# Performance work log

Measured on AMD Instinct MI355X. Metric: run time of the kernel, lower is better.

## Reference

```python
import jax, jax.numpy as jnp
import numpy as np

TOKEN = 40      # half window -> token_len D = 81
STRIDE = 4
NHEAD = 9
EPS = 1e-5
NEG = -1e30


def _tokenize(x):
    # x: [B, L] -> [B, S, D] centered sliding windows, zero padded
    B, L = x.shape
    D = 2 * TOKEN + 1
    S = -(-L // STRIDE)
    xp = jnp.pad(x, ((0, 0), (TOKEN, TOKEN)))
    idx = jnp.arange(S)[:, None] * STRIDE + jnp.arange(D)[None, :]
    return xp[:, idx]


def _pe(S, D):
    pos = jnp.arange(S, dtype=jnp.float32)[:, None]
    div = jnp.exp(-jnp.log(jnp.float32(10000.0)) * jnp.arange(0, D, 2, dtype=jnp.float32) / D)
    ang = pos * div  # [S, ceil(D/2)]
    pe = jnp.zeros((S, D), dtype=jnp.float32)
    pe = pe.at[:, 0::2].set(jnp.sin(ang))
    pe = pe.at[:, 1::2].set(jnp.cos(ang[:, : D // 2]))
    return pe


def _bn(x, g, b, axes):
    # training-mode batch norm over `axes`, channels last
    m = x.mean(axes, keepdims=True)
    v = x.var(axes, keepdims=True)
    return (x - m) / jnp.sqrt(v + EPS) * g + b


def _forward(x, basel, cali_spec, Wq, Wk, Wq2, Wk2, Wv2, Cv, Wo1, Wo2,
             corr_weight, h_weight, corr_map, g1, b1, ff1_w, ff1_b, g2, b2,
             ff2_w, ff2_b, g3, b3, token_v_w, token_v_b, beta1, alpha1, alpha2,
             fc1_w, fc1_b, bnf1_g, bnf1_b, fc2_w, fc2_b, bnf2_g, bnf2_b, fc3_w, fc3_b):
    D = 2 * TOKEN + 1
    dk = D // NHEAD
    # data normalization (load_data_scale semantics)
    xm = jnp.min(x[:, 20:-20])
    xs = jnp.abs(jnp.max(x[:, 20:-20] - xm))
    xn = (x - xm) / xs
    bs = basel[:, ::STRIDE]                      # [B, S]
    tx = _tokenize(xn)                           # [B, S, D]
    B, S, _ = tx.shape
    pe = _pe(S, D)
    tx = tx + pe
    cn = (cali_spec - xm) / xs
    tc = _tokenize(cn) + pe                      # [Bc, S, D]
    Bc = tc.shape[0]

    # ---- branch 2: calibration-spectrum attention over the batch dim ----
    Q2 = jnp.einsum('bse,hed->shbd', tx, Wq2)    # [S,H,B,dk]
    K2 = jnp.einsum('bse,hed->shbd', tx, Wk2)
    V2 = jnp.einsum('bse,hed->shbd', tx, Wv2)
    cK = jnp.einsum('cse,hed->shcd', tc, Wk2)    # [S,H,Bc,dk]
    cV = jnp.einsum('cse,hed->shcd', tc, Wv2)
    Kc = jnp.concatenate([K2, cK], axis=2)       # [S,H,B+Bc,dk]
    Vc = jnp.concatenate([V2, cV], axis=2)
    sc = jnp.einsum('shbd,shkd->shbk', Q2, Kc) / jnp.sqrt(jnp.float32(dk))
    cols = jnp.arange(B + Bc)
    # banded mask: each sample sees only itself among batch columns, all cali columns
    mask = (cols[None, :] >= B) | (cols[None, :] == jnp.arange(B)[:, None])  # [B, B+Bc]
    sc = jnp.where(mask[None, None], sc, NEG)
    A2 = jax.nn.softmax(sc, axis=-1)
    h2 = jnp.einsum('shbk,shkd->bshd', A2, Vc).reshape(B, S, D) @ Wo2  # [B,S,D]

    # ---- branch 1: correlation-map-biased attention over spectral positions ----
    xh = tx + h2
    Qs = jnp.einsum('bse,hed->bhsd', xh, Wq)
    Ks = jnp.einsum('bse,hed->bhsd', xh, Wk)
    Vs = jnp.einsum('bse,hed->bhsd', xh, Wq)     # original uses Wq for V (bug preserved)
    cw = corr_weight[0]
    bias = (corr_map @ Cv) / jnp.sqrt(jnp.float32(S))  # band_num == S
    As = (1.0 - cw) * jnp.einsum('bhsd,bhtd->bhst', Qs, Ks) / jnp.sqrt(jnp.float32(dk)) + cw * bias
    As = jax.nn.softmax(As, axis=-1)
    h1 = jnp.einsum('bhst,bhtd->bshd', As, Vs).reshape(B, S, D) @ Wo1
    hw = h_weight[0]
    att = (1.0 - hw) * h1 + hw * h2

    # ---- SpectrA residual + FF (BatchNorm over channels) ----
    ma = _bn(att + tx, g1, b1, (0, 1))
    f = jax.nn.relu(ma @ ff1_w + ff1_b)
    f = _bn(f, g2, b2, (0, 1))
    f = jax.nn.relu(f @ ff2_w + ff2_b)
    res = _bn(ma + f, g3, b3, (0, 1))

    # ---- ACiNet head ----
    a = (res @ token_v_w + token_v_b) * jax.nn.softmax(res @ beta1, axis=-1)
    a = a.sum(-1)                                # [B, S]
    fea = alpha1[0] * a + alpha2[0] * bs
    h = jax.nn.relu(fea @ fc1_w + fc1_b)
    h = _bn(h, bnf1_g, bnf1_b, (0,))
    h = jax.nn.relu(h @ fc2_w + fc2_b)
    h = _bn(h, bnf2_g, bnf2_b, (0,))
    return jnp.tanh(h @ fc3_w + fc3_b)


def setup_inputs() -> dict:
    key = jax.random.key(0)
    ks = iter(jax.random.split(key, 64))
    def rn(shape, s=0.05):
        return jax.random.normal(next(ks), shape, dtype=jnp.float32) * s
    B, Bc, L = 32, 16, 2048
    D, H, dk, S, FF, FC1, FC2, Y = 81, 9, 9, 512, 256, 512, 256, 4
    f32 = jnp.float32
    return {
        'x': rn((B, L), 1.0), 'basel': rn((B, L), 1.0), 'cali_spec': rn((Bc, L), 1.0),
        'Wq': rn((H, D, dk)), 'Wk': rn((H, D, dk)), 'Wq2': rn((H, D, dk)),
        'Wk2': rn((H, D, dk)), 'Wv2': rn((H, D, dk)),
        'Cv': rn((S, S)), 'Wo1': rn((D, D)), 'Wo2': rn((D, D)),
        'corr_weight': jnp.array([0.2], dtype=f32), 'h_weight': jnp.array([0.8], dtype=f32),
        'corr_map': rn((S, S), 1.0),
        'g1': jnp.ones(D, f32), 'b1': jnp.zeros(D, f32),
        'ff1_w': rn((D, FF)), 'ff1_b': jnp.zeros(FF, f32),
        'g2': jnp.ones(FF, f32), 'b2': jnp.zeros(FF, f32),
        'ff2_w': rn((FF, D)), 'ff2_b': jnp.zeros(D, f32),
        'g3': jnp.ones(D, f32), 'b3': jnp.zeros(D, f32),
        'token_v_w': rn((D, D)), 'token_v_b': jnp.zeros(D, f32),
        'beta1': jnp.ones((D, D), f32),
        'alpha1': jnp.array([0.8], dtype=f32), 'alpha2': jnp.array([0.2], dtype=f32),
        'fc1_w': rn((S, FC1)), 'fc1_b': jnp.zeros(FC1, f32),
        'bnf1_g': jnp.ones(FC1, f32), 'bnf1_b': jnp.zeros(FC1, f32),
        'fc2_w': rn((FC1, FC2)), 'fc2_b': jnp.zeros(FC2, f32),
        'bnf2_g': jnp.ones(FC2, f32), 'bnf2_b': jnp.zeros(FC2, f32),
        'fc3_w': rn((FC2, Y)), 'fc3_b': jnp.zeros(Y, f32),
    }


def reference(x, basel, cali_spec, Wq, Wk, Wq2, Wk2, Wv2, Cv, Wo1, Wo2,
              corr_weight, h_weight, corr_map, g1, b1, ff1_w, ff1_b, g2, b2,
              ff2_w, ff2_b, g3, b3, token_v_w, token_v_b, beta1, alpha1, alpha2,
              fc1_w, fc1_b, bnf1_g, bnf1_b, fc2_w, fc2_b, bnf2_g, bnf2_b, fc3_w, fc3_b):
    return _forward(x, basel, cali_spec, Wq, Wk, Wq2, Wk2, Wv2, Cv, Wo1, Wo2,
                    corr_weight, h_weight, corr_map, g1, b1, ff1_w, ff1_b, g2, b2,
                    ff2_w, ff2_b, g3, b3, token_v_w, token_v_b, beta1, alpha1, alpha2,
                    fc1_w, fc1_b, bnf1_g, bnf1_b, fc2_w, fc2_b, bnf2_g, bnf2_b, fc3_w, fc3_b)
```

## Files before the change

kernel.cpp:

```cpp
#include <hip/hip_runtime.h>
#include <hip/hip_bf16.h>
#include <math.h>

#define EPSV 1e-5f

typedef float vf2 __attribute__((ext_vector_type(2)));
typedef float vf4 __attribute__((ext_vector_type(4)));


__global__ void minmax_part(const float* __restrict__ x, float* __restrict__ part) {
    __shared__ float smin[256], smax[256];
    int tid = threadIdx.x;
    float mn = 1e30f, mx = -1e30f;
    for (int i = blockIdx.x * 256 + tid; i < 32 * 2008; i += 64 * 256) {
        int b = i / 2008, c = i % 2008 + 20;
        float v = x[b * 2048 + c];
        mn = fminf(mn, v); mx = fmaxf(mx, v);
    }
    smin[tid] = mn; smax[tid] = mx; __syncthreads();
    for (int off = 128; off > 0; off >>= 1) {
        if (tid < off) { smin[tid] = fminf(smin[tid], smin[tid + off]); smax[tid] = fmaxf(smax[tid], smax[tid + off]); }
        __syncthreads();
    }
    if (tid == 0) { part[blockIdx.x] = smin[0]; part[64 + blockIdx.x] = smax[0]; }
}

__global__ void minmax_fin(const float* __restrict__ part, float* __restrict__ scal) {
    __shared__ float smn[64], smx[64];
    int tid = threadIdx.x;
    smn[tid] = part[tid]; smx[tid] = part[64 + tid]; __syncthreads();
    for (int off = 32; off > 0; off >>= 1) {
        if (tid < off) { smn[tid] = fminf(smn[tid], smn[tid + off]); smx[tid] = fmaxf(smx[tid], smx[tid + off]); }
        __syncthreads();
    }
    if (tid == 0) { scal[0] = smn[0]; scal[1] = smx[0] - smn[0]; }
}

__global__ void pe_kernel(float* __restrict__ pe) {
    int idx = blockIdx.x * blockDim.x + threadIdx.x;
    if (idx >= 512 * 81) return;
    int d = idx % 81, s = idx / 81;
    int j = d >> 1;
    float dv = __expf(-9.210340371976184f * (2.0f * (float)j) / 81.0f);
    float ang = (float)s * dv;
    pe[idx] = (d & 1) ? cosf(ang) : sinf(ang);
}

__global__ void tokenize_kernel(const float* __restrict__ x, const float* __restrict__ cali,
                                const float* __restrict__ scal, const float* __restrict__ pe,
                                float* __restrict__ txall) {
    int idx = blockIdx.x * blockDim.x + threadIdx.x;
    if (idx >= 48 * 512 * 81) return;
    int d = idx % 81;
    int s = (idx / 81) % 512;
    int r = idx / (81 * 512);
    float xm = scal[0], inv_xs = 1.0f / scal[1];
    int oc = s * 4 + d - 40;
    float val = 0.0f;
    if (oc >= 0 && oc < 2048) {
        float sv = (r < 32) ? x[r * 2048 + oc] : cali[(r - 32) * 2048 + oc];
        val = (sv - xm) * inv_xs;
    }
    txall[idx] = val + pe[s * 81 + d];
}


__global__ __launch_bounds__(512) void qkv2_kernel(const float* __restrict__ txall,
                            const float* __restrict__ Wq2, const float* __restrict__ Wk2,
                            const float* __restrict__ Wv2,
                            float* __restrict__ Q2, float* __restrict__ Kc, float* __restrict__ Vc) {
    __shared__ float rows_[64 * 84];
    __shared__ float Wl[84 * 84];
    int blk = blockIdx.x;
    int t, rb;
    if (blk < 256)      { t = 0; rb = blk; }
    else if (blk < 640) { t = 1; rb = blk - 256; }
    else                { t = 2; rb = blk - 640; }
    int row0 = rb * 64;
    int k = row0 >> 9;
    int s0 = row0 & 511;
    const float* W = (t == 0) ? Wq2 : (t == 1) ? Wk2 : Wv2;
    int tid = threadIdx.x;
    for (int i = tid; i < 64 * 84; i += 512) {
        int c = i % 84;
        rows_[i] = (c < 81) ? txall[(row0 + i / 84) * 81 + c] : 0.0f;
    }
    for (int i = tid; i < 84 * 84; i += 512) {
        int e = i / 84, hd = i % 84;
        Wl[i] = (e < 81 && hd < 81) ? W[(hd / 9) * 729 + e * 9 + (hd % 9)] : 0.0f;
    }
    __syncthreads();
    for (int o = tid; o < 336; o += 512) {
        int r4 = o / 21, cg = o % 21;
        int c0 = cg * 4;
        const float* rp = rows_ + r4 * 4 * 84;
        vf4 acc0 = 0.0f, acc1 = 0.0f, acc2 = 0.0f, acc3 = 0.0f;
        #pragma unroll 7
        for (int e = 0; e < 84; e += 4) {
            vf4 w0 = *(const vf4*)(Wl + (e + 0) * 84 + c0);
            vf4 w1 = *(const vf4*)(Wl + (e + 1) * 84 + c0);
            vf4 w2 = *(const vf4*)(Wl + (e + 2) * 84 + c0);
            vf4 w3 = *(const vf4*)(Wl + (e + 3) * 84 + c0);
            vf4 r0 = *(const vf4*)(rp + e);
            vf4 r1 = *(const vf4*)(rp + 84 + e);
            vf4 r2 = *(const vf4*)(rp + 168 + e);
            vf4 r3 = *(const vf4*)(rp + 252 + e);
            acc0 += r0[0] * w0 + r0[1] * w1 + r0[2] * w2 + r0[3] * w3;
            acc1 += r1[0] * w0 + r1[1] * w1 + r1[2] * w2 + r1[3] * w3;
            acc2 += r2[0] * w0 + r2[1] * w1 + r2[2] * w2 + r2[3] * w3;
            acc3 += r3[0] * w0 + r3[1] * w1 + r3[2] * w2 + r3[3] * w3;
        }
        vf4 av[4] = {acc0, acc1, acc2, acc3};
        #pragma unroll
        for (int cc = 0; cc < 4; cc++) {
            int col = c0 + cc;
            if (col < 81) {
                int h = col / 9, d = col % 9;
                #pragma unroll
                for (int rr = 0; rr < 4; rr++) {
                    int s = s0 + r4 * 4 + rr;
                    if (t == 0)      Q2[((s * 9 + h) * 32 + k) * 9 + d] = av[rr][cc];
                    else if (t == 1) Kc[((s * 9 + h) * 48 + k) * 9 + d] = av[rr][cc];
                    else             Vc[((s * 9 + h) * 48 + k) * 9 + d] = av[rr][cc];
                }
            }
        }
    }
}

__global__ void attn2_kernel(const float* __restrict__ Q2, const float* __restrict__ Kc,
                             const float* __restrict__ Vc, float* __restrict__ tmp2) {
    int tid = blockIdx.x * blockDim.x + threadIdx.x;
    if (tid >= 512 * 9 * 32) return;
    int b = tid & 31;
    int h = (tid >> 5) % 9;
    int s = tid / 288;
    const float* q = Q2 + ((s * 9 + h) * 32 + b) * 9;
    float qr[9];
    const float c2 = 1.4426950408889634f / 3.0f;
    #pragma unroll
    for (int d = 0; d < 9; d++) qr[d] = q[d] * c2;
    const float* Kb = Kc + (s * 9 + h) * 48 * 9;
    const float* Vb = Vc + (s * 9 + h) * 48 * 9;
    float l = 0.0f, outv[9];
    #pragma unroll
    for (int d = 0; d < 9; d++) outv[d] = 0.0f;
    #pragma unroll
    for (int j = 0; j < 17; j++) {
        int k = (j == 0) ? b : 31 + j;
        const float* kp = Kb + k * 9;
        float acc = 0.0f;
        #pragma unroll
        for (int d = 0; d < 9; d++) acc += qr[d] * kp[d];
        float p = exp2f(acc);
        l += p;
        const float* vp = Vb + k * 9;
        #pragma unroll
        for (int d = 0; d < 9; d++) outv[d] += p * vp[d];
    }
    float invl = 1.0f / l;
    float* op = tmp2 + (b * 512 + s) * 81 + h * 9;
    #pragma unroll
    for (int d = 0; d < 9; d++) op[d] = outv[d] * invl;
}

__global__ __launch_bounds__(512) void h2xh_kernel(const float* __restrict__ tmp2,
                            const float* __restrict__ Wo2, const float* __restrict__ txall,
                            float* __restrict__ h2, float* __restrict__ xh) {
    __shared__ float rows_[64 * 84];
    __shared__ float Wl[84 * 84];
    int row0 = blockIdx.x * 64;
    int tid = threadIdx.x;
    for (int i = tid; i < 64 * 84; i += 512) {
        int c = i % 84;
        rows_[i] = (c < 81) ? tmp2[(row0 + i / 84) * 81 + c] : 0.0f;
    }
    for (int i = tid; i < 84 * 84; i += 512) {
        int e = i / 84, c = i % 84;
        Wl[i] = (e < 81 && c < 81) ? Wo2[e * 81 + c] : 0.0f;
    }
    __syncthreads();
    for (int o = tid; o < 336; o += 512) {
        int r4 = o / 21, cg = o % 21;
        int c0 = cg * 4;
        const float* rp = rows_ + r4 * 4 * 84;
        vf4 acc0 = 0.0f, acc1 = 0.0f, acc2 = 0.0f, acc3 = 0.0f;
        #pragma unroll 7
        for (int e = 0; e < 84; e += 4) {
            vf4 w0 = *(const vf4*)(Wl + (e + 0) * 84 + c0);
            vf4 w1 = *(const vf4*)(Wl + (e + 1) * 84 + c0);
            vf4 w2 = *(const vf4*)(Wl + (e + 2) * 84 + c0);
            vf4 w3 = *(const vf4*)(Wl + (e + 3) * 84 + c0);
            vf4 r0 = *(const vf4*)(rp + e);
            vf4 r1 = *(const vf4*)(rp + 84 + e);
            vf4 r2 = *(const vf4*)(rp + 168 + e);
            vf4 r3 = *(const vf4*)(rp + 252 + e);
            acc0 += r0[0] * w0 + r0[1] * w1 + r0[2] * w2 + r0[3] * w3;
            acc1 += r1[0] * w0 + r1[1] * w1 + r1[2] * w2 + r1[3] * w3;
            acc2 += r2[0] * w0 + r2[1] * w1 + r2[2] * w2 + r2[3] * w3;
            acc3 += r3[0] * w0 + r3[1] * w1 + r3[2] * w2 + r3[3] * w3;
        }
        vf4 av[4] = {acc0, acc1, acc2, acc3};
        #pragma unroll
        for (int cc = 0; cc < 4; cc++) {
            int col = c0 + cc;
            if (col < 81) {
                #pragma unroll
                for (int rr = 0; rr < 4; rr++) {
                    int idx = (row0 + r4 * 4 + rr) * 81 + col;
                    float v = av[rr][cc];
                    h2[idx] = v;
                    xh[idx] = txall[idx] + v;
                }
            }
        }
    }
}

__global__ __launch_bounds__(512) void qks_kernel(const float* __restrict__ xh,
                           const float* __restrict__ Wq, const float* __restrict__ Wk,
                           float* __restrict__ Qs, float* __restrict__ Ks) {
    __shared__ float rows_[64 * 84];
    __shared__ float Wl[84 * 84];
    int blk = blockIdx.x;
    int t = blk >> 8;
    int rb = blk & 255;
    int row0 = rb * 64;
    int b = row0 >> 9;
    int s0 = row0 & 511;
    const float* W = (t == 0) ? Wq : Wk;
    int tid = threadIdx.x;
    for (int i = tid; i < 64 * 84; i += 512) {
        int c = i % 84;
        rows_[i] = (c < 81) ? xh[(row0 + i / 84) * 81 + c] : 0.0f;
    }
    for (int i = tid; i < 84 * 84; i += 512) {
        int e = i / 84, hd = i % 84;
        Wl[i] = (e < 81 && hd < 81) ? W[(hd / 9) * 729 + e * 9 + (hd % 9)] : 0.0f;
    }
    __syncthreads();
    float* dst = (t == 0) ? Qs : Ks;
    for (int o = tid; o < 336; o += 512) {
        int r4 = o / 21, cg = o % 21;
        int c0 = cg * 4;
        const float* rp = rows_ + r4 * 4 * 84;
        vf4 acc0 = 0.0f, acc1 = 0.0f, acc2 = 0.0f, acc3 = 0.0f;
        #pragma unroll 7
        for (int e = 0; e < 84; e += 4) {
            vf4 w0 = *(const vf4*)(Wl + (e + 0) * 84 + c0);
            vf4 w1 = *(const vf4*)(Wl + (e + 1) * 84 + c0);
            vf4 w2 = *(const vf4*)(Wl + (e + 2) * 84 + c0);
            vf4 w3 = *(const vf4*)(Wl + (e + 3) * 84 + c0);
            vf4 r0 = *(const vf4*)(rp + e);
            vf4 r1 = *(const vf4*)(rp + 84 + e);
            vf4 r2 = *(const vf4*)(rp + 168 + e);
            vf4 r3 = *(const vf4*)(rp + 252 + e);
            acc0 += r0[0] * w0 + r0[1] * w1 + r0[2] * w2 + r0[3] * w3;
            acc1 += r1[0] * w0 + r1[1] * w1 + r1[2] * w2 + r1[3] * w3;
            acc2 += r2[0] * w0 + r2[1] * w1 + r2[2] * w2 + r2[3] * w3;
            acc3 += r3[0] * w0 + r3[1] * w1 + r3[2] * w2 + r3[3] * w3;
        }
        vf4 av[4] = {acc0, acc1, acc2, acc3};
        #pragma unroll
        for (int cc = 0; cc < 4; cc++) {
            int col = c0 + cc;
            if (col < 81) {
                int h = col / 9, d = col % 9;
                #pragma unroll
                for (int rr = 0; rr < 4; rr++)
                    dst[((b * 9 + h) * 512 + (s0 + r4 * 4 + rr)) * 9 + d] = av[rr][cc];
            }
        }
    }
}

__global__ __launch_bounds__(256) void biasmm_kernel(const float* __restrict__ corr,
                              const float* __restrict__ Cv, const float* __restrict__ cwp,
                              float* __restrict__ ebT) {
    __shared__ float As[32][33];
    __shared__ float Bs[32][33];
    int tx = threadIdx.x, ty = threadIdx.y;
    int tid = ty * 16 + tx;
    int t0 = blockIdx.y * 32, s0 = blockIdx.x * 32;
    float a00 = 0, a01 = 0, a10 = 0, a11 = 0;
    for (int k0 = 0; k0 < 512; k0 += 32) {
        for (int ii = tid; ii < 1024; ii += 256) {
            int r = ii >> 5, c = ii & 31;
            As[r][c] = Cv[(k0 + r) * 512 + t0 + c];
            Bs[r][c] = corr[(s0 + r) * 512 + k0 + c];
        }
        __syncthreads();
        #pragma unroll
        for (int kk = 0; kk < 32; kk++) {
            float b0 = Bs[tx][kk], b1 = Bs[tx + 16][kk];
            float c0 = As[kk][ty], c1 = As[kk][ty + 16];
            a00 += c0 * b0; a01 += c0 * b1; a10 += c1 * b0; a11 += c1 * b1;
        }
        __syncthreads();
    }
    float cws = cwp[0] * 0.04419417382415922f;
    ebT[(t0 + ty) * 512 + s0 + tx]            = __expf(a00 * cws);
    ebT[(t0 + ty) * 512 + s0 + tx + 16]       = __expf(a01 * cws);
    ebT[(t0 + ty + 16) * 512 + s0 + tx]       = __expf(a10 * cws);
    ebT[(t0 + ty + 16) * 512 + s0 + tx + 16]  = __expf(a11 * cws);
}

__global__ __launch_bounds__(256) void attn1_kernel(const float* __restrict__ Qs,
                                                    const float* __restrict__ Ks,
                                                    const float* __restrict__ ebT,
                                                    const float* __restrict__ cwp,
                                                    float* __restrict__ part) {
    int blk = blockIdx.x;
    int bh = blk >> 4;
    int qhalf = (blk >> 3) & 1;
    int kq8 = blk & 7;
    int tid = threadIdx.x;
    const float* Kb = Ks + bh * 4608;
    const float* Qb = Qs + bh * 4608;
    int q = qhalf * 256 + tid;
    float c1 = (1.0f - cwp[0]) * (1.4426950408889634f / 3.0f);
    vf2 qv[4];
    float q8;
    {
        const float* qp = Qb + q * 9;
        #pragma unroll
        for (int d = 0; d < 4; d++) {
            vf2 t; t.x = c1 * qp[2 * d]; t.y = c1 * qp[2 * d + 1];
            qv[d] = t;
        }
        q8 = c1 * qp[8];
    }
    float l = 0.0f, a8 = 0.0f;
    vf2 acc[4];
    #pragma unroll
    for (int d = 0; d < 4; d++) acc[d] = (vf2)0.0f;
    int k0 = kq8 * 64;
    const float* ebp = ebT + q;
    for (int t0 = k0; t0 < k0 + 64; t0 += 8) {
        float eb[8];
        #pragma unroll
        for (int j = 0; j < 8; j++) eb[j] = ebp[(t0 + j) << 9];
        #pragma unroll
        for (int j = 0; j < 8; j++) {
            const float* kr = Kb + (t0 + j) * 9;
            const float* vr = Qb + (t0 + j) * 9;
            vf2 k0v; k0v.x = kr[0]; k0v.y = kr[1];
            vf2 k1v; k1v.x = kr[2]; k1v.y = kr[3];
            vf2 k2v; k2v.x = kr[4]; k2v.y = kr[5];
            vf2 k3v; k3v.x = kr[6]; k3v.y = kr[7];
            vf2 u2 = qv[0] * k0v + qv[1] * k1v + qv[2] * k2v + qv[3] * k3v;
            float u = u2.x + u2.y + q8 * kr[8];
            float p = exp2f(u) * eb[j];
            l += p;
            vf2 p2; p2.x = p; p2.y = p;
            vf2 v0; v0.x = vr[0]; v0.y = vr[1];
            vf2 v1; v1.x = vr[2]; v1.y = vr[3];
            vf2 v2; v2.x = vr[4]; v2.y = vr[5];
            vf2 v3; v3.x = vr[6]; v3.y = vr[7];
            acc[0] += p2 * v0; acc[1] += p2 * v1;
            acc[2] += p2 * v2; acc[3] += p2 * v3;
            a8 += p * vr[8];
        }
    }
    int gidx = bh * 512 + q;
    atomicAdd(&part[gidx], l);
    #pragma unroll
    for (int d = 0; d < 4; d++) {
        atomicAdd(&part[(1 + 2 * d) * 147456 + gidx], acc[d].x);
        atomicAdd(&part[(2 + 2 * d) * 147456 + gidx], acc[d].y);
    }
    atomicAdd(&part[9 * 147456 + gidx], a8);
}

__global__ __launch_bounds__(512) void h1o_kernel(const float* __restrict__ apart,
                           const float* __restrict__ Wo1, const float* __restrict__ h2,
                           const float* __restrict__ txall, const float* __restrict__ hwp,
                           float* __restrict__ matin, float* __restrict__ st1) {
    __shared__ float rows_[64 * 84];
    __shared__ float Wl[84 * 84];
    __shared__ float ssum[81], ssq[81];
    int row0 = blockIdx.x * 64;
    int tid = threadIdx.x;
    if (tid < 81) { ssum[tid] = 0.0f; ssq[tid] = 0.0f; }
    for (int i = tid; i < 64 * 84; i += 512) {
        int r = i / 84, c = i % 84;
        float v = 0.0f;
        if (c < 81) {
            int row = row0 + r;
            int b = row >> 9, s = row & 511;
            int h = c / 9, d = c % 9;
            int gidx = (b * 9 + h) * 512 + s;
            float L = apart[gidx];
            float A = apart[(1 + d) * 147456 + gidx];
            v = A / L;
        }
        rows_[i] = v;
    }
    for (int i = tid; i < 84 * 84; i += 512) {
        int e = i / 84, c = i % 84;
        Wl[i] = (e < 81 && c < 81) ? Wo1[e * 81 + c] : 0.0f;
    }
    __syncthreads();
    float hw = hwp[0];
    float onemhw = 1.0f - hw;
    for (int o = tid; o < 336; o += 512) {
        int r4 = o / 21, cg = o % 21;
        int c0 = cg * 4;
        const float* rp = rows_ + r4 * 4 * 84;
        vf4 acc0 = 0.0f, acc1 = 0.0f, acc2 = 0.0f, acc3 = 0.0f;
        #pragma unroll 7
        for (int e = 0; e < 84; e += 4) {
            vf4 w0 = *(const vf4*)(Wl + (e + 0) * 84 + c0);
            vf4 w1 = *(const vf4*)(Wl + (e + 1) * 84 + c0);
            vf4 w2 = *(const vf4*)(Wl + (e + 2) * 84 + c0);
            vf4 w3 = *(const vf4*)(Wl + (e + 3) * 84 + c0);
            vf4 r0 = *(const vf4*)(rp + e);
            vf4 r1 = *(const vf4*)(rp + 84 + e);
            vf4 r2 = *(const vf4*)(rp + 168 + e);
            vf4 r3 = *(const vf4*)(rp + 252 + e);
            acc0 += r0[0] * w0 + r0[1] * w1 + r0[2] * w2 + r0[3] * w3;
            acc1 += r1[0] * w0 + r1[1] * w1 + r1[2] * w2 + r1[3] * w3;
            acc2 += r2[0] * w0 + r2[1] * w1 + r2[2] * w2 + r2[3] * w3;
            acc3 += r3[0] * w0 + r3[1] * w1 + r3[2] * w2 + r3[3] * w3;
        }
        vf4 av[4] = {acc0, acc1, acc2, acc3};
        #pragma unroll
        for (int cc = 0; cc < 4; cc++) {
            int col = c0 + cc;
            if (col < 81) {
                float ls = 0.0f, lq = 0.0f;
                #pragma unroll
                for (int rr = 0; rr < 4; rr++) {
                    int idx = (row0 + r4 * 4 + rr) * 81 + col;
                    float v = onemhw * av[rr][cc] + hw * h2[idx] + txall[idx];
                    matin[idx] = v;
                    ls += v; lq += v * v;
                }
                atomicAdd(&ssum[col], ls);
                atomicAdd(&ssq[col], lq);
            }
        }
    }
    __syncthreads();
    if (tid < 81) {
        atomicAdd(&st1[tid], ssum[tid]);
        atomicAdd(&st1[81 + tid], ssq[tid]);
    }
}

__global__ __launch_bounds__(512) void ff1_kernel(const float* __restrict__ matin,
                           const float* __restrict__ st1, const float* __restrict__ g1,
                           const float* __restrict__ b1, const float* __restrict__ W,
                           const float* __restrict__ bias, float* __restrict__ f1,
                           float* __restrict__ st2) {
    __shared__ float rows_[64 * 84];
    __shared__ float Wl[84 * 64];
    __shared__ float s2s[64], s2q[64];
    int row0 = blockIdx.x * 64;
    int cb = blockIdx.y * 64;
    int tid = threadIdx.x;
    const float invN = 1.0f / 16384.0f;
    if (tid < 64) { s2s[tid] = 0.0f; s2q[tid] = 0.0f; }
    for (int i = tid; i < 64 * 84; i += 512) {
        int c = i % 84;
        float v = 0.0f;
        if (c < 81) {
            float mean = st1[c] * invN;
            float var = st1[81 + c] * invN - mean * mean;
            v = (matin[(row0 + i / 84) * 81 + c] - mean) * rsqrtf(var + EPSV) * g1[c] + b1[c];
        }
        rows_[i] = v;
    }
    for (int i = tid; i < 84 * 64; i += 512) {
        int e = i >> 6, cc = i & 63;
        Wl[i] = (e < 81) ? W[e * 256 + cb + cc] : 0.0f;
    }
    __syncthreads();
    if (tid < 256) {
        int o = tid;
        int r4 = o >> 4, cg = o & 15;
        int c0 = cg * 4;
        const float* rp = rows_ + r4 * 4 * 84;
        vf4 acc0 = 0.0f, acc1 = 0.0f, acc2 = 0.0f, acc3 = 0.0f;
        #pragma unroll 7
        for (int e = 0; e < 84; e += 4) {
            vf4 w0 = *(const vf4*)(Wl + ((e + 0) << 6) + c0);
            vf4 w1 = *(const vf4*)(Wl + ((e + 1) << 6) + c0);
            vf4 w2 = *(const vf4*)(Wl + ((e + 2) << 6) + c0);
            vf4 w3 = *(const vf4*)(Wl + ((e + 3) << 6) + c0);
            vf4 r0 = *(const vf4*)(rp + e);
            vf4 r1 = *(const vf4*)(rp + 84 + e);
            vf4 r2 = *(const vf4*)(rp + 168 + e);
            vf4 r3 = *(const vf4*)(rp + 252 + e);
            acc0 += r0[0] * w0 + r0[1] * w1 + r0[2] * w2 + r0[3] * w3;
            acc1 += r1[0] * w0 + r1[1] * w1 + r1[2] * w2 + r1[3] * w3;
            acc2 += r2[0] * w0 + r2[1] * w1 + r2[2] * w2 + r2[3] * w3;
            acc3 += r3[0] * w0 + r3[1] * w1 + r3[2] * w2 + r3[3] * w3;
        }
        vf4 bv = *(const vf4*)(bias + cb + c0);
        acc0 = __builtin_elementwise_max(acc0 + bv, (vf4)0.0f);
        acc1 = __builtin_elementwise_max(acc1 + bv, (vf4)0.0f);
        acc2 = __builtin_elementwise_max(acc2 + bv, (vf4)0.0f);
        acc3 = __builtin_elementwise_max(acc3 + bv, (vf4)0.0f);
        int base = (row0 + r4 * 4) * 256 + cb + c0;
        *(vf4*)(f1 + base)       = acc0;
        *(vf4*)(f1 + base + 256) = acc1;
        *(vf4*)(f1 + base + 512) = acc2;
        *(vf4*)(f1 + base + 768) = acc3;
        vf4 cs = acc0 + acc1 + acc2 + acc3;
        vf4 cq = acc0 * acc0 + acc1 * acc1 + acc2 * acc2 + acc3 * acc3;
        #pragma unroll
        for (int cc = 0; cc < 4; cc++) {
            atomicAdd(&s2s[c0 + cc], cs[cc]);
            atomicAdd(&s2q[c0 + cc], cq[cc]);
        }
    }
    __syncthreads();
    if (tid < 64) {
        atomicAdd(&st2[cb + tid], s2s[tid]);
        atomicAdd(&st2[256 + cb + tid], s2q[tid]);
    }
}

__global__ __launch_bounds__(512) void ff2_kernel(const float* __restrict__ f1,
                           const float* __restrict__ st2, const float* __restrict__ g2,
                           const float* __restrict__ b2, const float* __restrict__ W,
                           const float* __restrict__ bias, const float* __restrict__ matin,
                           const float* __restrict__ st1, const float* __restrict__ g1,
                           const float* __restrict__ b1, float* __restrict__ t3,
                           float* __restrict__ st3) {
    __shared__ float rows_[32 * 68];
    __shared__ float Wl[64 * 84];
    __shared__ float s3s[81], s3q[81];
    int row0 = blockIdx.x * 32;
    int tid = threadIdx.x;
    const float invN = 1.0f / 16384.0f;
    if (tid < 81) { s3s[tid] = 0.0f; s3q[tid] = 0.0f; }
    int o = tid;
    int r4 = o / 21, cg = o % 21;
    int c0 = cg * 4;
    bool active = (o < 168);
    vf4 acc0 = 0.0f, acc1 = 0.0f, acc2 = 0.0f, acc3 = 0.0f;
    for (int kq = 0; kq < 4; kq++) {
        __syncthreads();
        for (int i = tid; i < 32 * 68; i += 512) {
            int r = i / 68, e = i % 68;
            float v = 0.0f;
            if (e < 64) {
                int c = kq * 64 + e;
                float mean = st2[c] * invN;
                float var = st2[256 + c] * invN - mean * mean;
                v = (f1[(row0 + r) * 256 + c] - mean) * rsqrtf(var + EPSV) * g2[c] + b2[c];
            }
            rows_[i] = v;
        }
        for (int i = tid; i < 64 * 84; i += 512) {
            int e = i / 84, c = i % 84;
            Wl[i] = (c < 81) ? W[(kq * 64 + e) * 81 + c] : 0.0f;
        }
        __syncthreads();
        if (active) {
            const float* rp = rows_ + r4 * 4 * 68;
            #pragma unroll 8
            for (int e = 0; e < 64; e += 4) {
                vf4 w0 = *(const vf4*)(Wl + (e + 0) * 84 + c0);
                vf4 w1 = *(const vf4*)(Wl + (e + 1) * 84 + c0);
                vf4 w2 = *(const vf4*)(Wl + (e + 2) * 84 + c0);
                vf4 w3 = *(const vf4*)(Wl + (e + 3) * 84 + c0);
                vf4 r0 = *(const vf4*)(rp + e);
                vf4 r1 = *(const vf4*)(rp + 68 + e);
                vf4 r2 = *(const vf4*)(rp + 136 + e);
                vf4 r3 = *(const vf4*)(rp + 204 + e);
                acc0 += r0[0] * w0 + r0[1] * w1 + r0[2] * w2 + r0[3] * w3;
                acc1 += r1[0] * w0 + r1[1] * w1 + r1[2] * w2 + r1[3] * w3;
                acc2 += r2[0] * w0 + r2[1] * w1 + r2[2] * w2 + r2[3] * w3;
                acc3 += r3[0] * w0 + r3[1] * w1 + r3[2] * w2 + r3[3] * w3;
            }
        }
    }
    if (active) {
        vf4 av[4] = {acc0, acc1, acc2, acc3};
        #pragma unroll
        for (int cc = 0; cc < 4; cc++) {
            int col = c0 + cc;
            if (col < 81) {
                float mean = st1[col] * invN;
                float var = st1[81 + col] * invN - mean * mean;
                float rstd = rsqrtf(var + EPSV);
                float bval = bias[col];
                float ls = 0.0f, lq = 0.0f;
                #pragma unroll
                for (int rr = 0; rr < 4; rr++) {
                    int idx = (row0 + r4 * 4 + rr) * 81 + col;
                    float ma = (matin[idx] - mean) * rstd * g1[col] + b1[col];
                    float v = ma + fmaxf(av[rr][cc] + bval, 0.0f);
                    t3[idx] = v;
                    ls += v; lq += v * v;
                }
                atomicAdd(&s3s[col], ls);
                atomicAdd(&s3q[col], lq);
            }
        }
    }
    __syncthreads();
    if (tid < 81) {
        atomicAdd(&st3[tid], s3s[tid]);
        atomicAdd(&st3[81 + tid], s3q[tid]);
    }
}

__global__ __launch_bounds__(512) void token_mm(const float* __restrict__ t3,
                            const float* __restrict__ st3, const float* __restrict__ g3,
                            const float* __restrict__ b3, const float* __restrict__ tvw,
                            const float* __restrict__ beta1,
                            float* __restrict__ uv0, float* __restrict__ uv1) {
    __shared__ float rows_[64 * 84];
    __shared__ float Wl[84 * 84];
    int blk = blockIdx.x;
    int t = blk >> 8;
    int row0 = (blk & 255) * 64;
    const float* W = (t == 0) ? tvw : beta1;
    float* dst = (t == 0) ? uv0 : uv1;
    int tid = threadIdx.x;
    const float invN = 1.0f / 16384.0f;
    for (int i = tid; i < 64 * 84; i += 512) {
        int c = i % 84;
        float v = 0.0f;
        if (c < 81) {
            float mean = st3[c] * invN;
            float var = st3[81 + c] * invN - mean * mean;
            v = (t3[(row0 + i / 84) * 81 + c] - mean) * rsqrtf(var + EPSV) * g3[c] + b3[c];
        }
        rows_[i] = v;
    }
    for (int i = tid; i < 84 * 84; i += 512) {
        int e = i / 84, c = i % 84;
        Wl[i] = (e < 81 && c < 81) ? W[e * 81 + c] : 0.0f;
    }
    __syncthreads();
    for (int o = tid; o < 336; o += 512) {
        int r4 = o / 21, cg = o % 21;
        int c0 = cg * 4;
        const float* rp = rows_ + r4 * 4 * 84;
        vf4 acc0 = 0.0f, acc1 = 0.0f, acc2 = 0.0f, acc3 = 0.0f;
        #pragma unroll 7
        for (int e = 0; e < 84; e += 4) {
            vf4 w0 = *(const vf4*)(Wl + (e + 0) * 84 + c0);
            vf4 w1 = *(const vf4*)(Wl + (e + 1) * 84 + c0);
            vf4 w2 = *(const vf4*)(Wl + (e + 2) * 84 + c0);
            vf4 w3 = *(const vf4*)(Wl + (e + 3) * 84 + c0);
            vf4 r0 = *(const vf4*)(rp + e);
            vf4 r1 = *(const vf4*)(rp + 84 + e);
            vf4 r2 = *(const vf4*)(rp + 168 + e);
            vf4 r3 = *(const vf4*)(rp + 252 + e);
            acc0 += r0[0] * w0 + r0[1] * w1 + r0[2] * w2 + r0[3] * w3;
            acc1 += r1[0] * w0 + r1[1] * w1 + r1[2] * w2 + r1[3] * w3;
            acc2 += r2[0] * w0 + r2[1] * w1 + r2[2] * w2 + r2[3] * w3;
            acc3 += r3[0] * w0 + r3[1] * w1 + r3[2] * w2 + r3[3] * w3;
        }
        vf4 av[4] = {acc0, acc1, acc2, acc3};
        #pragma unroll
        for (int cc = 0; cc < 4; cc++) {
            int col = c0 + cc;
            if (col < 81) {
                #pragma unroll
                for (int rr = 0; rr < 4; rr++)
                    dst[(row0 + r4 * 4 + rr) * 81 + col] = av[rr][cc];
            }
        }
    }
}

__global__ __launch_bounds__(256) void token_pool(const float* __restrict__ uv0,
                             const float* __restrict__ uv1, const float* __restrict__ tvb,
                             const float* __restrict__ basel, const float* __restrict__ a1p,
                             const float* __restrict__ a2p, float* __restrict__ fea) {
    int tid = threadIdx.x;
    int r = tid >> 3, j = tid & 7;
    int row = blockIdx.x * 32 + r;
    int base = row * 81;
    float u[11], v[11];
    #pragma unroll
    for (int dd = 0; dd < 11; dd++) {
        int d = j + dd * 8;
        if (d < 81) {
            u[dd] = uv0[base + d] + tvb[d];
            v[dd] = uv1[base + d];
        } else {
            u[dd] = 0.0f; v[dd] = -1e30f;
        }
    }
    float mx = -1e30f;
    #pragma unroll
    for (int dd = 0; dd < 11; dd++) mx = fmaxf(mx, v[dd]);
    #pragma unroll
    for (int msk = 1; msk < 8; msk <<= 1) mx = fmaxf(mx, __shfl_xor(mx, msk, 8));
    float sp = 0.0f, sup = 0.0f;
    #pragma unroll
    for (int dd = 0; dd < 11; dd++) {
        float p = __expf(v[dd] - mx);
        sp += p; sup += u[dd] * p;
    }
    #pragma unroll
    for (int msk = 1; msk < 8; msk <<= 1) {
        sp  += __shfl_xor(sp, msk, 8);
        sup += __shfl_xor(sup, msk, 8);
    }
    if (j == 0) {
        int b = row >> 9, s = row & 511;
        fea[row] = a1p[0] * (sup / sp) + a2p[0] * basel[b * 2048 + s * 4];
    }
}

__global__ void fc1_kernel(const float* __restrict__ in, const float* __restrict__ W,
                           const float* __restrict__ bias, float* __restrict__ out,
                           float* __restrict__ st) {
    int idx = blockIdx.x * blockDim.x + threadIdx.x;
    if (idx >= 32 * 512) return;
    int b = idx >> 9, j = idx & 511;
    float acc = bias[j];
    const float* ip = in + (b << 9);
    #pragma unroll 8
    for (int k = 0; k < 512; k++) acc += ip[k] * W[k * 512 + j];
    acc = fmaxf(acc, 0.0f);
    out[idx] = acc;
    atomicAdd(&st[j], acc);
    atomicAdd(&st[512 + j], acc * acc);
}

__global__ __launch_bounds__(256) void fc2_kernel(const float* __restrict__ in,
                           const float* __restrict__ st4, const float* __restrict__ g,
                           const float* __restrict__ bb, const float* __restrict__ W,
                           const float* __restrict__ bias, float* __restrict__ out,
                           float* __restrict__ st5) {
    __shared__ float scale[512], shift[512];
    int tid = threadIdx.x;
    for (int k = tid; k < 512; k += 256) {
        float mean = st4[k] * (1.0f / 32.0f);
        float var = st4[512 + k] * (1.0f / 32.0f) - mean * mean;
        float sc_ = rsqrtf(var + EPSV) * g[k];
        scale[k] = sc_;
        shift[k] = bb[k] - mean * sc_;
    }
    __syncthreads();
    int idx = blockIdx.x * 256 + tid;
    if (idx >= 32 * 256) return;
    int b = idx >> 8, j = idx & 255;
    float acc = bias[j];
    const float* ip = in + (b << 9);
    #pragma unroll 8
    for (int k = 0; k < 512; k++) acc += (ip[k] * scale[k] + shift[k]) * W[k * 256 + j];
    acc = fmaxf(acc, 0.0f);
    out[idx] = acc;
    atomicAdd(&st5[j], acc);
    atomicAdd(&st5[256 + j], acc * acc);
}

__global__ void fc3_kernel(const float* __restrict__ in, const float* __restrict__ st5,
                           const float* __restrict__ g, const float* __restrict__ bb,
                           const float* __restrict__ W, const float* __restrict__ bias,
                           float* __restrict__ out) {
    __shared__ float scale[256], shift[256];
    int tid = threadIdx.x;
    for (int k = tid; k < 256; k += 128) {
        float mean = st5[k] * (1.0f / 32.0f);
        float var = st5[256 + k] * (1.0f / 32.0f) - mean * mean;
        float sc_ = rsqrtf(var + EPSV) * g[k];
        scale[k] = sc_;
        shift[k] = bb[k] - mean * sc_;
    }
    __syncthreads();
    int b = tid >> 2, j = tid & 3;
    float acc = bias[j];
    const float* ip = in + (b << 8);
    #pragma unroll 8
    for (int k = 0; k < 256; k++) acc += (ip[k] * scale[k] + shift[k]) * W[k * 4 + j];
    out[tid] = tanhf(acc);
}

extern "C" void kernel_launch(void* const* d_in, const int* in_sizes, int n_in,
                              void* d_out, int out_size, void* d_ws, size_t ws_size,
                              hipStream_t stream) {
    const float* x       = (const float*)d_in[0];
    const float* basel   = (const float*)d_in[1];
    const float* cali    = (const float*)d_in[2];
    const float* Wq      = (const float*)d_in[3];
    const float* Wk      = (const float*)d_in[4];
    const float* Wq2     = (const float*)d_in[5];
    const float* Wk2     = (const float*)d_in[6];
    const float* Wv2     = (const float*)d_in[7];
    const float* Cv      = (const float*)d_in[8];
    const float* Wo1     = (const float*)d_in[9];
    const float* Wo2     = (const float*)d_in[10];
    const float* corr_w  = (const float*)d_in[11];
    const float* h_w     = (const float*)d_in[12];
    const float* corr    = (const float*)d_in[13];
    const float* g1      = (const float*)d_in[14];
    const float* b1      = (const float*)d_in[15];
    const float* ff1_w   = (const float*)d_in[16];
    const float* ff1_b   = (const float*)d_in[17];
    const float* g2      = (const float*)d_in[18];
    const float* b2      = (const float*)d_in[19];
    const float* ff2_w   = (const float*)d_in[20];
    const float* ff2_b   = (const float*)d_in[21];
    const float* g3      = (const float*)d_in[22];
    const float* b3      = (const float*)d_in[23];
    const float* tvw     = (const float*)d_in[24];
    const float* tvb     = (const float*)d_in[25];
    const float* beta1   = (const float*)d_in[26];
    const float* a1      = (const float*)d_in[27];
    const float* a2      = (const float*)d_in[28];
    const float* fc1_w   = (const float*)d_in[29];
    const float* fc1_b   = (const float*)d_in[30];
    const float* bnf1_g  = (const float*)d_in[31];
    const float* bnf1_b  = (const float*)d_in[32];
    const float* fc2_w   = (const float*)d_in[33];
    const float* fc2_b   = (const float*)d_in[34];
    const float* bnf2_g  = (const float*)d_in[35];
    const float* bnf2_b  = (const float*)d_in[36];
    const float* fc3_w   = (const float*)d_in[37];
    const float* fc3_b   = (const float*)d_in[38];
    float* out = (float*)d_out;
    float* ws = (float*)d_ws;

    const size_t SCAL  = 0;
    const size_t PART  = 16;
    const size_t ST1   = 512;
    const size_t ST2   = 768;
    const size_t ST3   = 1536;
    const size_t ST4   = 1792;
    const size_t ST5   = 2880;
    const size_t FEA   = 4096;
    const size_t FCH1  = 20480;
    const size_t FCH2  = 36864;
    const size_t PEO   = 45056;
    const size_t TX    = 90112;
    const size_t Q2O   = 2080768;
    const size_t KCO   = 3407872;
    const size_t VCO   = 5398528;
    const size_t TMP2  = 7389184;
    const size_t H2O   = 8716288;
    const size_t XHO   = 10043392;
    const size_t BIASO = 11370496;
    const size_t F1O   = 11632640;

    float* scal  = ws + SCAL;
    float* part  = ws + PART;
    float* st1   = ws + ST1;
    float* st2   = ws + ST2;
    float* st3   = ws + ST3;
    float* st4   = ws + ST4;
    float* st5   = ws + ST5;
    float* fea   = ws + FEA;
    float* fch1  = ws + FCH1;
    float* fch2  = ws + FCH2;
    float* pe    = ws + PEO;
    float* txall = ws + TX;
    float* Q2    = ws + Q2O;
    float* Kc    = ws + KCO;
    float* Vc    = ws + VCO;
    float* tmp2  = ws + TMP2;
    float* h2    = ws + H2O;
    float* xh    = ws + XHO;
    float* ebT   = ws + BIASO;
    float* f1    = ws + F1O;
    float* Qs    = Kc;
    float* Ks    = Vc;
    float* matin = tmp2;
    float* t3    = h2;
    float* apart = f1;
    float* uv0   = tmp2;
    float* uv1   = xh;

    hipMemsetAsync(ws, 0, 4096 * sizeof(float), stream);
    hipMemsetAsync(apart, 0, 1474560 * sizeof(float), stream);

    minmax_part<<<64, 256, 0, stream>>>(x, part);
    minmax_fin<<<1, 64, 0, stream>>>(part, scal);

    pe_kernel<<<(512 * 81 + 255) / 256, 256, 0, stream>>>(pe);

    tokenize_kernel<<<(48 * 512 * 81 + 255) / 256, 256, 0, stream>>>(x, cali, scal, pe, txall);

    qkv2_kernel<<<1024, 512, 0, stream>>>(txall, Wq2, Wk2, Wv2, Q2, Kc, Vc);

    attn2_kernel<<<(512 * 9 * 32) / 256, 256, 0, stream>>>(Q2, Kc, Vc, tmp2);

    h2xh_kernel<<<256, 512, 0, stream>>>(tmp2, Wo2, txall, h2, xh);

    qks_kernel<<<512, 512, 0, stream>>>(xh, Wq, Wk, Qs, Ks);

    biasmm_kernel<<<dim3(16, 16), dim3(16, 16), 0, stream>>>(corr, Cv, corr_w, ebT);

    attn1_kernel<<<4608, 256, 0, stream>>>(Qs, Ks, ebT, corr_w, apart);

    h1o_kernel<<<256, 512, 0, stream>>>(apart, Wo1, h2, txall, h_w, matin, st1);

    ff1_kernel<<<dim3(256, 4), 512, 0, stream>>>(matin, st1, g1, b1, ff1_w, ff1_b, f1, st2);

    ff2_kernel<<<512, 512, 0, stream>>>(f1, st2, g2, b2, ff2_w, ff2_b,
                                        matin, st1, g1, b1, t3, st3);

    token_mm<<<512, 512, 0, stream>>>(t3, st3, g3, b3, tvw, beta1, uv0, uv1);
    token_pool<<<512, 256, 0, stream>>>(uv0, uv1, tvb, basel, a1, a2, fea);

    fc1_kernel<<<64, 256, 0, stream>>>(fea, fc1_w, fc1_b, fch1, st4);

    fc2_kernel<<<32, 256, 0, stream>>>(fch1, st4, bnf1_g, bnf1_b, fc2_w, fc2_b, fch2, st5);

    fc3_kernel<<<1, 128, 0, stream>>>(fch2, st5, bnf2_g, bnf2_b, fc3_w, fc3_b, out);
}
```

Before: 403.3 us.

## Fuse minmax finalize and PE into tokenize, fuse attn2 into h2xh

Folds the final min/max reduction and the positional-encoding computation into the tokenize kernel, so each block reduces the 64 partials itself and computes sin/cos inline. The branch-2 attention is computed directly inside h2xh into shared memory, which removes the tmp2 round trip and two kernel launches. In exchange, every tokenize block redundantly reduces the partials and evaluates transcendentals, and h2xh has only 576 attention tasks per 512-thread block, so some threads do two passes.

```diff
diff --git a/kernel.cpp b/kernel.cpp
--- a/kernel.cpp
+++ b/kernel.cpp
@@ -25,43 +25,39 @@
     if (tid == 0) { part[blockIdx.x] = smin[0]; part[64 + blockIdx.x] = smax[0]; }
 }
 
-__global__ void minmax_fin(const float* __restrict__ part, float* __restrict__ scal) {
-    __shared__ float smn[64], smx[64];
-    int tid = threadIdx.x;
-    smn[tid] = part[tid]; smx[tid] = part[64 + tid]; __syncthreads();
-    for (int off = 32; off > 0; off >>= 1) {
-        if (tid < off) { smn[tid] = fminf(smn[tid], smn[tid + off]); smx[tid] = fmaxf(smx[tid], smx[tid + off]); }
-        __syncthreads();
-    }
-    if (tid == 0) { scal[0] = smn[0]; scal[1] = smx[0] - smn[0]; }
-}
-
-__global__ void pe_kernel(float* __restrict__ pe) {
-    int idx = blockIdx.x * blockDim.x + threadIdx.x;
-    if (idx >= 512 * 81) return;
-    int d = idx % 81, s = idx / 81;
-    int j = d >> 1;
-    float dv = __expf(-9.210340371976184f * (2.0f * (float)j) / 81.0f);
-    float ang = (float)s * dv;
-    pe[idx] = (d & 1) ? cosf(ang) : sinf(ang);
-}
-
 __global__ void tokenize_kernel(const float* __restrict__ x, const float* __restrict__ cali,
-                                const float* __restrict__ scal, const float* __restrict__ pe,
-                                float* __restrict__ txall) {
-    int idx = blockIdx.x * blockDim.x + threadIdx.x;
+                                const float* __restrict__ part, float* __restrict__ txall) {
+    __shared__ float scal2[2];
+    int tid = threadIdx.x;
+    if (tid == 0) {
+        float mn = part[0];
+        #pragma unroll 8
+        for (int i = 1; i < 64; i++) mn = fminf(mn, part[i]);
+        scal2[0] = mn;
+    } else if (tid == 64) {
+        float mx = part[64];
+        #pragma unroll 8
+        for (int i = 65; i < 128; i++) mx = fmaxf(mx, part[i]);
+        scal2[1] = mx;
+    }
+    __syncthreads();
+    int idx = blockIdx.x * blockDim.x + tid;
     if (idx >= 48 * 512 * 81) return;
     int d = idx % 81;
     int s = (idx / 81) % 512;
     int r = idx / (81 * 512);
-    float xm = scal[0], inv_xs = 1.0f / scal[1];
+    float xm = scal2[0], inv_xs = 1.0f / (scal2[1] - scal2[0]);
     int oc = s * 4 + d - 40;
     float val = 0.0f;
     if (oc >= 0 && oc < 2048) {
         float sv = (r < 32) ? x[r * 2048 + oc] : cali[(r - 32) * 2048 + oc];
         val = (sv - xm) * inv_xs;
     }
-    txall[idx] = val + pe[s * 81 + d];
+    int j = d >> 1;
+    float dv = __expf(-9.210340371976184f * (2.0f * (float)j) / 81.0f);
+    float ang = (float)s * dv;
+    float pe = (d & 1) ? cosf(ang) : sinf(ang);
+    txall[idx] = val + pe;
 }
 
 
@@ -128,56 +124,51 @@
     }
 }
 
-__global__ void attn2_kernel(const float* __restrict__ Q2, const float* __restrict__ Kc,
-                             const float* __restrict__ Vc, float* __restrict__ tmp2) {
-    int tid = blockIdx.x * blockDim.x + threadIdx.x;
-    if (tid >= 512 * 9 * 32) return;
-    int b = tid & 31;
-    int h = (tid >> 5) % 9;
-    int s = tid / 288;
-    const float* q = Q2 + ((s * 9 + h) * 32 + b) * 9;
-    float qr[9];
-    const float c2 = 1.4426950408889634f / 3.0f;
-    #pragma unroll
-    for (int d = 0; d < 9; d++) qr[d] = q[d] * c2;
-    const float* Kb = Kc + (s * 9 + h) * 48 * 9;
-    const float* Vb = Vc + (s * 9 + h) * 48 * 9;
-    float l = 0.0f, outv[9];
-    #pragma unroll
-    for (int d = 0; d < 9; d++) outv[d] = 0.0f;
-    #pragma unroll
-    for (int j = 0; j < 17; j++) {
-        int k = (j == 0) ? b : 31 + j;
-        const float* kp = Kb + k * 9;
-        float acc = 0.0f;
-        #pragma unroll
-        for (int d = 0; d < 9; d++) acc += qr[d] * kp[d];
-        float p = exp2f(acc);
-        l += p;
-        const float* vp = Vb + k * 9;
-        #pragma unroll
-        for (int d = 0; d < 9; d++) outv[d] += p * vp[d];
-    }
-    float invl = 1.0f / l;
-    float* op = tmp2 + (b * 512 + s) * 81 + h * 9;
-    #pragma unroll
-    for (int d = 0; d < 9; d++) op[d] = outv[d] * invl;
-}
-
-__global__ __launch_bounds__(512) void h2xh_kernel(const float* __restrict__ tmp2,
+__global__ __launch_bounds__(512) void h2xh_kernel(const float* __restrict__ Q2,
+                            const float* __restrict__ Kc, const float* __restrict__ Vc,
                             const float* __restrict__ Wo2, const float* __restrict__ txall,
                             float* __restrict__ h2, float* __restrict__ xh) {
     __shared__ float rows_[64 * 84];
     __shared__ float Wl[84 * 84];
     int row0 = blockIdx.x * 64;
-    int tid = threadIdx.x;
-    for (int i = tid; i < 64 * 84; i += 512) {
-        int c = i % 84;
-        rows_[i] = (c < 81) ? tmp2[(row0 + i / 84) * 81 + c] : 0.0f;
-    }
+    int b = row0 >> 9, s0 = row0 & 511;
+    int tid = threadIdx.x;
     for (int i = tid; i < 84 * 84; i += 512) {
         int e = i / 84, c = i % 84;
         Wl[i] = (e < 81 && c < 81) ? Wo2[e * 81 + c] : 0.0f;
+    }
+    for (int o = tid; o < 192; o += 512)
+        rows_[(o / 3) * 84 + 81 + (o % 3)] = 0.0f;
+    const float c2 = 1.4426950408889634f / 3.0f;
+    for (int o = tid; o < 576; o += 512) {
+        int sl = o / 9, h = o % 9;
+        int s = s0 + sl;
+        const float* q = Q2 + ((s * 9 + h) * 32 + b) * 9;
+        float qr[9];
+        #pragma unroll
+        for (int d = 0; d < 9; d++) qr[d] = q[d] * c2;
+        const float* Kb = Kc + (s * 9 + h) * 432;
+        const float* Vb = Vc + (s * 9 + h) * 432;
+        float l = 0.0f, outv[9];
+        #pragma unroll
+        for (int d = 0; d < 9; d++) outv[d] = 0.0f;
+        #pragma unroll
+        for (int j = 0; j < 17; j++) {
+            int k = (j == 0) ? b : 31 + j;
+            const float* kp = Kb + k * 9;
+            float acc = 0.0f;
+            #pragma unroll
+            for (int d = 0; d < 9; d++) acc += qr[d] * kp[d];
+            float p = exp2f(acc);
+            l += p;
+            const float* vp = Vb + k * 9;
+            #pragma unroll
+            for (int d = 0; d < 9; d++) outv[d] += p * vp[d];
+        }
+        float invl = 1.0f / l;
+        float* op = rows_ + sl * 84 + h * 9;
+        #pragma unroll
+        for (int d = 0; d < 9; d++) op[d] = outv[d] * invl;
     }
     __syncthreads();
     for (int o = tid; o < 336; o += 512) {
@@ -823,7 +814,6 @@
     float* out = (float*)d_out;
     float* ws = (float*)d_ws;
 
-    const size_t SCAL  = 0;
     const size_t PART  = 16;
     const size_t ST1   = 512;
     const size_t ST2   = 768;
@@ -833,7 +823,6 @@
     const size_t FEA   = 4096;
     const size_t FCH1  = 20480;
     const size_t FCH2  = 36864;
-    const size_t PEO   = 45056;
     const size_t TX    = 90112;
     const size_t Q2O   = 2080768;
     const size_t KCO   = 3407872;
@@ -844,7 +833,6 @@
     const size_t BIASO = 11370496;
     const size_t F1O   = 11632640;
 
-    float* scal  = ws + SCAL;
     float* part  = ws + PART;
     float* st1   = ws + ST1;
     float* st2   = ws + ST2;
@@ -854,7 +842,6 @@
     float* fea   = ws + FEA;
     float* fch1  = ws + FCH1;
     float* fch2  = ws + FCH2;
-    float* pe    = ws + PEO;
     float* txall = ws + TX;
     float* Q2    = ws + Q2O;
     float* Kc    = ws + KCO;
@@ -876,17 +863,12 @@
     hipMemsetAsync(apart, 0, 1474560 * sizeof(float), stream);
 
     minmax_part<<<64, 256, 0, stream>>>(x, part);
-    minmax_fin<<<1, 64, 0, stream>>>(part, scal);
-
-    pe_kernel<<<(512 * 81 + 255) / 256, 256, 0, stream>>>(pe);
-
-    tokenize_kernel<<<(48 * 512 * 81 + 255) / 256, 256, 0, stream>>>(x, cali, scal, pe, txall);
+
+    tokenize_kernel<<<(48 * 512 * 81 + 255) / 256, 256, 0, stream>>>(x, cali, part, txall);
 
     qkv2_kernel<<<1024, 512, 0, stream>>>(txall, Wq2, Wk2, Wv2, Q2, Kc, Vc);
 
-    attn2_kernel<<<(512 * 9 * 32) / 256, 256, 0, stream>>>(Q2, Kc, Vc, tmp2);
-
-    h2xh_kernel<<<256, 512, 0, stream>>>(tmp2, Wo2, txall, h2, xh);
+    h2xh_kernel<<<256, 512, 0, stream>>>(Q2, Kc, Vc, Wo2, txall, h2, xh);
 
     qks_kernel<<<512, 512, 0, stream>>>(xh, Wq, Wk, Qs, Ks);
 
```

New measurement: 440.5 us, median of 2. +9.2%, slower.
